# Kernel optimization log

Measured on AMD Instinct MI355X. Metric: run time of the kernel, lower is better.

## Reference

```python
import jax, jax.numpy as jnp
import numpy as np

COL = 14
NJ = 23
SIGMA = 1.0
RADIUS = int(4.0 * SIGMA + 0.5)  # scipy gaussian_filter default truncate=4.0


def _gauss_matrix(col=COL, sigma=SIGMA, radius=RADIUS):
    """col x col matrix M such that (M @ img @ M.T) == scipy gaussian_filter(img, sigma)
    with scipy's default 'reflect' boundary (== numpy 'symmetric')."""
    xs = np.arange(-radius, radius + 1)
    w = np.exp(-0.5 * (xs / sigma) ** 2)
    w = (w / w.sum()).astype(np.float32)
    M = np.zeros((col, col), np.float32)
    for out in range(col):
        for k in range(-radius, radius + 1):
            i = (out + k) % (2 * col)
            if i >= col:
                i = 2 * col - 1 - i
            M[out, i] += w[k + radius]
    return M

_M = jnp.asarray(_gauss_matrix())


def setup_inputs() -> dict:
    key = jax.random.key(0)
    k0, k1, k2, k3 = jax.random.split(key, 4)
    B = 4096
    o = jax.random.normal(k0, (B, 3 * NJ, COL, COL), dtype=jnp.float32)
    h = jax.random.uniform(k1, (B, NJ, COL, COL), dtype=jnp.float32)
    t = jax.random.uniform(k2, (B, NJ, 3), dtype=jnp.float32)
    v = jax.random.randint(k3, (B, NJ, 2), 0, 2, dtype=jnp.int32)
    return {"o": o, "h": h, "t": t, "v": v}


def reference(o, h, t, v):
    B = h.shape[0]
    scale = 1.0 / COL

    # per-joint argmax over the heatmap -> integer (y, x) coords
    idx = jnp.argmax(h.reshape(B, NJ, COL * COL), axis=-1)  # [B, Nj]
    y = idx // COL
    x = idx % COL

    bi = jnp.arange(B)[:, None]
    ji = jnp.arange(NJ)[None, :]
    px = o[bi, ji, y, x] + x.astype(h.dtype) * scale
    py = o[bi, ji + NJ, y, x] + y.astype(h.dtype) * scale
    pz = o[bi, ji + 2 * NJ, y, x]
    pred = jnp.stack([px, py, pz], axis=-1)  # [B, Nj, 3]

    # target heatmaps: delta at (yi, xi), gaussian-filtered, min-max normalized
    ti = t * COL
    xi = jnp.trunc(ti[..., 0]).astype(jnp.int32)  # int() truncation as in torch code
    yi = jnp.trunc(ti[..., 1]).astype(jnp.int32)
    in_range = (xi >= 0) & (xi <= COL - 1) & (yi >= 0) & (yi <= COL - 1)
    mask = (v[..., 0] == 1) & in_range  # [B, Nj]

    xc = jnp.clip(xi, 0, COL - 1)
    yc = jnp.clip(yi, 0, COL - 1)
    # gaussian_filter of a one-hot delta is the outer product of two filter columns
    gy = _M.T[yc]  # [B, Nj, COL], gy[..., r] = M[r, yc]
    gx = _M.T[xc]  # [B, Nj, COL]
    tt_map = gy[..., :, None] * gx[..., None, :]  # [B, Nj, COL, COL]
    mn = tt_map.min(axis=(-2, -1), keepdims=True)
    mx = tt_map.max(axis=(-2, -1), keepdims=True)
    tt = (tt_map - mn) / (mx - mn)
    tt = tt * mask[..., None, None].astype(h.dtype)

    d1 = jnp.sum((h - tt) ** 2) / NJ
    d2 = jnp.sum((pred - t) ** 2) / NJ
    return d1 + d2
```

## Files before the change

### kernel.cpp

```cpp
#include <hip/hip_runtime.h>
#include <math.h>

#define COL 14
#define NJ 23
#define BATCH 4096
#define NJOINT (BATCH * NJ)
#define RADIUS 4
#define BLOCKS 1024
#define THREADS 256
#define WAVES_TOTAL (BLOCKS * (THREADS / 64))
#define JOINTS_PER_WAVE (NJOINT / WAVES_TOTAL)

__global__ __launch_bounds__(THREADS) void msq3d_kernel(
    const float* __restrict__ o,
    const float* __restrict__ h,
    const float* __restrict__ t,
    const int*   __restrict__ v,
    float* __restrict__ out)
{
    __shared__ float sM[COL][COL];
    __shared__ float sColMin[COL], sColMax[COL];
    __shared__ float sWaveSum[THREADS / 64];

    const int tid = threadIdx.x;

    if (tid < COL * COL) {
        double wd[2 * RADIUS + 1];
        double wsum = 0.0;
        #pragma unroll
        for (int k = 0; k <= 2 * RADIUS; ++k) {
            double xx = (double)(k - RADIUS);
            wd[k] = exp(-0.5 * xx * xx);
            wsum += wd[k];
        }
        const int outr = tid / COL, ic = tid % COL;
        float acc = 0.0f;
        #pragma unroll
        for (int k = -RADIUS; k <= RADIUS; ++k) {
            int ii = (outr + k) % (2 * COL);
            if (ii < 0) ii += 2 * COL;
            if (ii >= COL) ii = 2 * COL - 1 - ii;
            if (ii == ic) acc += (float)(wd[k + RADIUS] / wsum);
        }
        sM[outr][ic] = acc;
    }
    __syncthreads();
    if (tid < COL) {
        float mn = sM[0][tid], mx = mn;
        for (int r = 1; r < COL; ++r) {
            float x = sM[r][tid];
            mn = fminf(mn, x);
            mx = fmaxf(mx, x);
        }
        sColMin[tid] = mn;
        sColMax[tid] = mx;
    }
    __syncthreads();

    const int lane = tid & 63;
    const int wave_in_blk = tid >> 6;
    const int gwave = blockIdx.x * (THREADS / 64) + wave_in_blk;
    const float scale = 1.0f / (float)COL;

    float accD = 0.0f;

    const int jbase = gwave * JOINTS_PER_WAVE;
    for (int jj = 0; jj < JOINTS_PER_WAVE; ++jj) {
        const int joint = jbase + jj;
        const int b = joint / NJ;
        const int j = joint - b * NJ;

        const float t0 = t[joint * 3 + 0];
        const float t1 = t[joint * 3 + 1];
        const float t2 = t[joint * 3 + 2];
        const int   v0 = v[joint * 2 + 0];

        const float tx = t0 * (float)COL;
        const float ty = t1 * (float)COL;
        const int xi = (int)truncf(tx);
        const int yi = (int)truncf(ty);
        const bool in_range = (xi >= 0) && (xi <= COL - 1) && (yi >= 0) && (yi <= COL - 1);
        const bool mask = (v0 == 1) && in_range;
        const int xc = min(max(xi, 0), COL - 1);
        const int yc = min(max(yi, 0), COL - 1);

        const float mn = sColMin[yc] * sColMin[xc];
        const float mx = sColMax[yc] * sColMax[xc];
        const float inv = 1.0f / (mx - mn);
        const float fm = mask ? 1.0f : 0.0f;

        const float* hb = h + (size_t)joint * (COL * COL);
        float bestv = -INFINITY;
        int besti = 0;

        #pragma unroll
        for (int pass = 0; pass < 4; ++pass) {
            int p = pass * 64 + lane;
            if (p < COL * COL) {
                float hv = hb[p];
                if (hv > bestv) { bestv = hv; besti = p; }
                int r = p / COL;
                int c = p - r * COL;
                float ttv = fm * ((sM[r][yc] * sM[c][xc]) - mn) * inv;
                float d = hv - ttv;
                accD += d * d;
            }
        }

        #pragma unroll
        for (int off = 32; off > 0; off >>= 1) {
            float ov = __shfl_down(bestv, off, 64);
            int   oi = __shfl_down(besti, off, 64);
            if (ov > bestv || (ov == bestv && oi < besti)) { bestv = ov; besti = oi; }
        }

        if (lane == 0) {
            const int y = besti / COL;
            const int x = besti - y * COL;
            const size_t ob = (((size_t)b * (3 * NJ) + j) * COL + y) * COL + x;
            const float o0 = o[ob];
            const float o1 = o[ob + (size_t)NJ * COL * COL];
            const float o2 = o[ob + (size_t)(2 * NJ) * COL * COL];
            const float px = o0 + (float)x * scale;
            const float py = o1 + (float)y * scale;
            const float dx = px - t0;
            const float dy = py - t1;
            const float dz = o2 - t2;
            accD += dx * dx + dy * dy + dz * dz;
        }
    }

    #pragma unroll
    for (int off = 32; off > 0; off >>= 1)
        accD += __shfl_down(accD, off, 64);
    if (lane == 0) sWaveSum[wave_in_blk] = accD;
    __syncthreads();
    if (tid == 0) {
        float s = 0.0f;
        #pragma unroll
        for (int w = 0; w < THREADS / 64; ++w) s += sWaveSum[w];
        atomicAdd(out, s * (1.0f / (float)NJ));
    }
}

extern "C" void kernel_launch(void* const* d_in, const int* in_sizes, int n_in,
                              void* d_out, int out_size, void* d_ws, size_t ws_size,
                              hipStream_t stream) {
    const float* o = (const float*)d_in[0];
    const float* h = (const float*)d_in[1];
    const float* t = (const float*)d_in[2];
    const int*   v = (const int*)d_in[3];
    float* out = (float*)d_out;

    hipMemsetAsync(d_out, 0, sizeof(float), stream);
    msq3d_kernel<<<BLOCKS, THREADS, 0, stream>>>(o, h, t, v, out);
}
```

Measured before the change: 340.8 us.

## Vectorize heatmap loads as float4 and use ballot-based argmax reduction

Each lane now loads four contiguous heatmap values with one float4 load, which replaces four strided scalar passes. The argmax reduction becomes a float max butterfly followed by a ballot and ffs to pick the lowest-index winner, in place of a paired value/index shuffle reduction. Masked-off joints skip building the target map and accumulate h squared directly. The grid doubles to 2048 blocks, and joints are assigned grid-strided instead of as contiguous chunks per wave. The float4 load relies on each 196-float joint being 16-byte aligned, which holds because 196*4 bytes is a multiple of 16.

```diff
diff --git a/kernel.cpp b/kernel.cpp
--- a/kernel.cpp
+++ b/kernel.cpp
@@ -6,10 +6,9 @@
 #define BATCH 4096
 #define NJOINT (BATCH * NJ)
 #define RADIUS 4
-#define BLOCKS 1024
 #define THREADS 256
+#define BLOCKS 2048
 #define WAVES_TOTAL (BLOCKS * (THREADS / 64))
-#define JOINTS_PER_WAVE (NJOINT / WAVES_TOTAL)
 
 __global__ __launch_bounds__(THREADS) void msq3d_kernel(
     const float* __restrict__ o,
@@ -18,7 +17,7 @@
     const int*   __restrict__ v,
     float* __restrict__ out)
 {
-    __shared__ float sM[COL][COL];
+    __shared__ float sM[COL * COL];
     __shared__ float sColMin[COL], sColMax[COL];
     __shared__ float sWaveSum[THREADS / 64];
 
@@ -42,13 +41,13 @@
             if (ii >= COL) ii = 2 * COL - 1 - ii;
             if (ii == ic) acc += (float)(wd[k + RADIUS] / wsum);
         }
-        sM[outr][ic] = acc;
+        sM[outr * COL + ic] = acc;
     }
     __syncthreads();
     if (tid < COL) {
-        float mn = sM[0][tid], mx = mn;
+        float mn = sM[tid], mx = mn;
         for (int r = 1; r < COL; ++r) {
-            float x = sM[r][tid];
+            float x = sM[r * COL + tid];
             mn = fminf(mn, x);
             mx = fmaxf(mx, x);
         }
@@ -62,11 +61,20 @@
     const int gwave = blockIdx.x * (THREADS / 64) + wave_in_blk;
     const float scale = 1.0f / (float)COL;
 
+    const bool act = (lane < 49);
+    const int q0 = lane * 4;
+    int rk[4], ck[4];
+    #pragma unroll
+    for (int k = 0; k < 4; ++k) {
+        int q = q0 + k;
+        if (q > COL * COL - 1) q = COL * COL - 1;
+        rk[k] = q / COL;
+        ck[k] = q - rk[k] * COL;
+    }
+
     float accD = 0.0f;
 
-    const int jbase = gwave * JOINTS_PER_WAVE;
-    for (int jj = 0; jj < JOINTS_PER_WAVE; ++jj) {
-        const int joint = jbase + jj;
+    for (int joint = gwave; joint < NJOINT; joint += WAVES_TOTAL) {
         const int b = joint / NJ;
         const int j = joint - b * NJ;
 
@@ -75,44 +83,52 @@
         const float t2 = t[joint * 3 + 2];
         const int   v0 = v[joint * 2 + 0];
 
-        const float tx = t0 * (float)COL;
-        const float ty = t1 * (float)COL;
-        const int xi = (int)truncf(tx);
-        const int yi = (int)truncf(ty);
+        const int xi = (int)truncf(t0 * (float)COL);
+        const int yi = (int)truncf(t1 * (float)COL);
         const bool in_range = (xi >= 0) && (xi <= COL - 1) && (yi >= 0) && (yi <= COL - 1);
         const bool mask = (v0 == 1) && in_range;
         const int xc = min(max(xi, 0), COL - 1);
         const int yc = min(max(yi, 0), COL - 1);
 
-        const float mn = sColMin[yc] * sColMin[xc];
-        const float mx = sColMax[yc] * sColMax[xc];
-        const float inv = 1.0f / (mx - mn);
-        const float fm = mask ? 1.0f : 0.0f;
+        const float4* hb4 = (const float4*)(h + (size_t)joint * (COL * COL));
+        float4 hv4 = make_float4(0.f, 0.f, 0.f, 0.f);
+        if (act) hv4 = hb4[lane];
+        const float hv[4] = {hv4.x, hv4.y, hv4.z, hv4.w};
 
-        const float* hb = h + (size_t)joint * (COL * COL);
-        float bestv = -INFINITY;
-        int besti = 0;
-
-        #pragma unroll
-        for (int pass = 0; pass < 4; ++pass) {
-            int p = pass * 64 + lane;
-            if (p < COL * COL) {
-                float hv = hb[p];
-                if (hv > bestv) { bestv = hv; besti = p; }
-                int r = p / COL;
-                int c = p - r * COL;
-                float ttv = fm * ((sM[r][yc] * sM[c][xc]) - mn) * inv;
-                float d = hv - ttv;
-                accD += d * d;
+        float lv = -INFINITY;
+        int   lq = 0;
+        if (act) {
+            #pragma unroll
+            for (int k = 0; k < 4; ++k) {
+                if (hv[k] > lv) { lv = hv[k]; lq = q0 + k; }
             }
         }
 
+        if (mask) {
+            const float mn  = sColMin[yc] * sColMin[xc];
+            const float mx  = sColMax[yc] * sColMax[xc];
+            const float inv = 1.0f / (mx - mn);
+            if (act) {
+                #pragma unroll
+                for (int k = 0; k < 4; ++k) {
+                    float ttv = (sM[rk[k] * COL + yc] * sM[ck[k] * COL + xc] - mn) * inv;
+                    float d = hv[k] - ttv;
+                    accD += d * d;
+                }
+            }
+        } else if (act) {
+            #pragma unroll
+            for (int k = 0; k < 4; ++k)
+                accD += hv[k] * hv[k];
+        }
+
+        float wmax = lv;
         #pragma unroll
-        for (int off = 32; off > 0; off >>= 1) {
-            float ov = __shfl_down(bestv, off, 64);
-            int   oi = __shfl_down(besti, off, 64);
-            if (ov > bestv || (ov == bestv && oi < besti)) { bestv = ov; besti = oi; }
-        }
+        for (int off = 1; off < 64; off <<= 1)
+            wmax = fmaxf(wmax, __shfl_xor(wmax, off, 64));
+        unsigned long long mb = __ballot(act && (lv == wmax));
+        const int src = (int)(__ffsll((long long)mb) - 1);
+        const int besti = __shfl(lq, src, 64);
 
         if (lane == 0) {
             const int y = besti / COL;
@@ -121,10 +137,8 @@
             const float o0 = o[ob];
             const float o1 = o[ob + (size_t)NJ * COL * COL];
             const float o2 = o[ob + (size_t)(2 * NJ) * COL * COL];
-            const float px = o0 + (float)x * scale;
-            const float py = o1 + (float)y * scale;
-            const float dx = px - t0;
-            const float dy = py - t1;
+            const float dx = (o0 + (float)x * scale) - t0;
+            const float dy = (o1 + (float)y * scale) - t1;
             const float dz = o2 - t2;
             accD += dx * dx + dy * dy + dz * dz;
         }
```

Measured after the change: 326.9 us. 4.1% less time.
